# Kernel optimization log

Measured on AMD Instinct MI355X. Metric: run time of the kernel, lower is better.

The kernel has to match this reference:

```python
import jax, jax.numpy as jnp
import numpy as np

N = 100000   # nodes
E = 1600000  # edges (before self-loops)
IN, H, HID, OUT = 128, 4, 32, 16
G, NPG = 100, 1000  # graphs, nodes per graph
NEG_SLOPE = 0.2


def setup_inputs() -> dict:
    key = jax.random.key(0)
    ks = jax.random.split(key, 12)
    x = jax.random.normal(ks[0], (N, IN), dtype=jnp.float32)
    # node type in column 0: first node of each graph is the root (type 0)
    node_type = (jnp.arange(N) % NPG != 0).astype(jnp.float32)
    x = x.at[:, 0].set(node_type)
    edge_index = jax.random.randint(ks[1], (2, E), 0, N, dtype=jnp.int64)
    batch = (jnp.arange(N) // NPG).astype(jnp.int64)
    s = 0.1
    W1 = jax.random.normal(ks[2], (IN, H * HID), dtype=jnp.float32) * s
    att_src1 = jax.random.normal(ks[3], (H, HID), dtype=jnp.float32) * s
    att_dst1 = jax.random.normal(ks[4], (H, HID), dtype=jnp.float32) * s
    bias1 = jnp.zeros((H * HID,), dtype=jnp.float32)
    W2 = jax.random.normal(ks[5], (H * HID, OUT), dtype=jnp.float32) * s
    att_src2 = jax.random.normal(ks[6], (1, OUT), dtype=jnp.float32) * s
    att_dst2 = jax.random.normal(ks[7], (1, OUT), dtype=jnp.float32) * s
    bias2 = jnp.zeros((OUT,), dtype=jnp.float32)
    return {"x": x, "edge_index": edge_index, "batch": batch,
            "W1": W1, "att_src1": att_src1, "att_dst1": att_dst1, "bias1": bias1,
            "W2": W2, "att_src2": att_src2, "att_dst2": att_dst2, "bias2": bias2}


def gat_conv(x, src, dst, W, att_src, att_dst, bias, heads, out_ch, concat):
    n = x.shape[0]
    h = (x @ W).reshape(n, heads, out_ch)           # [N,H,C]
    a_src = jnp.einsum('nhc,hc->nh', h, att_src)    # [N,H]
    a_dst = jnp.einsum('nhc,hc->nh', h, att_dst)
    e = a_src[src] + a_dst[dst]                     # [E',H]
    e = jnp.where(e > 0, e, NEG_SLOPE * e)          # leaky_relu(0.2)
    # segment softmax over incoming edges of each dst node
    m = jax.ops.segment_max(e, dst, num_segments=n)
    e = jnp.exp(e - m[dst])
    denom = jax.ops.segment_sum(e, dst, num_segments=n)
    alpha = e / (denom[dst] + 1e-16)                # [E',H]
    msg = h[src] * alpha[:, :, None]                # [E',H,C]
    out = jax.ops.segment_sum(msg, dst, num_segments=n)  # [N,H,C]
    if concat:
        return out.reshape(n, heads * out_ch) + bias
    return out.mean(axis=1) + bias


def reference(x, edge_index, batch, W1, att_src1, att_dst1, bias1,
              W2, att_src2, att_dst2, bias2):
    # eval mode: feature/attention dropout are identity
    ar = jnp.arange(N, dtype=edge_index.dtype)
    ei = jnp.concatenate([edge_index, jnp.stack([ar, ar])], axis=1)  # add self-loops
    src, dst = ei[0], ei[1]
    h = gat_conv(x, src, dst, W1, att_src1, att_dst1, bias1, H, HID, True)
    h = jax.nn.elu(h)
    out = gat_conv(h, src, dst, W2, att_src2, att_dst2, bias2, 1, OUT, False)
    # first root (node_type==0) per graph
    node_types = x[:, 0]
    cand = jnp.where(node_types == 0, jnp.arange(N), N)
    roots = jax.ops.segment_min(cand, batch, num_segments=G)
    return out[roots]
```

## Files before the change

kernel.cpp:

```cpp
#include <hip/hip_runtime.h>
#include <math.h>

#define NN 100000
#define EE 1600000
#define GG 100
#define DIN 128
#define F1 128
#define FOUT 16

#define C1CAP 16384
#define C0CAP 49152
#define L2CAP 32768
#define DEGCAP 128
#define NT 16

#define O_CNT      0
#define O_FLAG1    (O_CNT + 8)
#define O_FLAG0    (O_FLAG1 + NN)
#define O_ISROOT   (O_FLAG0 + NN)
#define O_FILL     (O_ISROOT + NN)
#define O_ZEND     (O_FILL + C1CAP)
#define O_ROOT     (O_ZEND)
#define O_MAP1     (O_ROOT + GG)
#define O_MAP0     (O_MAP1 + NN)
#define O_LIST1    (O_MAP0 + NN)
#define O_LIST0    (O_LIST1 + C1CAP)
#define O_L2       (O_LIST0 + C0CAP)
#define O_ORDER    (O_L2 + L2CAP*2)
#define O_H1       (O_ORDER + C1CAP*DEGCAP)
#define O_A1S      (O_H1 + C0CAP*F1)
#define O_A1D      (O_A1S + C0CAP*4)
#define O_H2       (O_A1D + C0CAP*4)
#define O_A2S      (O_H2 + C1CAP*FOUT)
#define O_A2D      (O_A2S + C1CAP)
#define O_END      (O_A2D + C1CAP)

__global__ __launch_bounds__(256) void gat_roots(
    const float* __restrict__ x, const int* __restrict__ batch, int* ws) {
  int i = blockIdx.x * blockDim.x + threadIdx.x;
  if (i < NN && x[(size_t)i * DIN] == 0.f)
    atomicMin((unsigned int*)&ws[O_ROOT + batch[i]], (unsigned int)i);
  __threadfence();
  __syncthreads();
  __shared__ int lastFlag;
  if (threadIdx.x == 0)
    lastFlag = (atomicAdd(&ws[O_CNT + 7], 1) == (int)gridDim.x - 1);
  __syncthreads();
  if (!lastFlag) return;
  int g = threadIdx.x;
  if (g >= GG) return;
  unsigned int r = __hip_atomic_load((unsigned int*)&ws[O_ROOT + g],
                                     __ATOMIC_ACQUIRE, __HIP_MEMORY_SCOPE_AGENT);
  if (r >= NN) return;
  ws[O_ISROOT + r] = g + 1;
  ws[O_FLAG1 + r] = 1;
  int idx = atomicAdd(&ws[O_CNT + 0], 1);
  if (idx < C1CAP) {
    ws[O_MAP1 + r] = idx;
    ws[O_LIST1 + idx] = r;
    ws[O_FILL + idx] = 1;
    ws[O_ORDER + idx * DEGCAP] = (int)r;
  }
  int p = atomicAdd(&ws[O_CNT + 3], 1);
  if (p < L2CAP) { ws[O_L2 + 2*p] = (int)r; ws[O_L2 + 2*p + 1] = g; }
  ws[O_FLAG0 + r] = 1;
  int i0 = atomicAdd(&ws[O_CNT + 1], 1);
  if (i0 < C0CAP) { ws[O_MAP0 + r] = i0; ws[O_LIST0 + i0] = (int)r; }
}

#define SB2 1600
__global__ __launch_bounds__(256) void gat_scan2(const int* __restrict__ ei, int* __restrict__ ws) {
  __shared__ int sp[SB2 * 2];
  __shared__ int sc[SB2];
  __shared__ int nP, nC, bP, bC, b0;
  if (threadIdx.x == 0) { nP = 0; nC = 0; }
  __syncthreads();
  const int perBlock = (EE + gridDim.x - 1) / gridDim.x;
  const int beg = blockIdx.x * perBlock;
  const int end = min(beg + perBlock, EE);
  for (int e = beg + threadIdx.x; e < end; e += 256) {
    int d = ei[EE + e];
    int gi = ws[O_ISROOT + d];
    if (gi) {
      int s = ei[e];
      int p = atomicAdd(&nP, 1);
      sp[2*p] = s; sp[2*p + 1] = gi - 1;
      if (atomicCAS(&ws[O_FLAG1 + s], 0, 1) == 0)
        sc[atomicAdd(&nC, 1)] = s;
    }
  }
  __syncthreads();
  if (threadIdx.x == 0) {
    bP = nP ? atomicAdd(&ws[O_CNT + 3], nP) : 0;
    bC = nC ? atomicAdd(&ws[O_CNT + 0], nC) : 0;
    b0 = nC ? atomicAdd(&ws[O_CNT + 1], nC) : 0;
  }
  __syncthreads();
  for (int i = threadIdx.x; i < nP; i += 256) {
    int p = bP + i;
    if (p < L2CAP) { ws[O_L2 + 2*p] = sp[2*i]; ws[O_L2 + 2*p + 1] = sp[2*i + 1]; }
  }
  for (int i = threadIdx.x; i < nC; i += 256) {
    int node = sc[i], idx = bC + i, i0 = b0 + i;
    if (idx < C1CAP) {
      ws[O_MAP1 + node] = idx;
      ws[O_LIST1 + idx] = node;
      ws[O_FILL + idx] = 1;
      ws[O_ORDER + idx * DEGCAP] = node;
    }
    ws[O_FLAG0 + node] = 1;
    if (i0 < C0CAP) { ws[O_MAP0 + node] = i0; ws[O_LIST0 + i0] = node; }
  }
}

__global__ __launch_bounds__(256) void gat_scan1(const int* __restrict__ ei, int* __restrict__ ws) {
  __shared__ int sc[SB2];
  __shared__ int nC, b0;
  if (threadIdx.x == 0) nC = 0;
  __syncthreads();
  const int perBlock = (EE + gridDim.x - 1) / gridDim.x;
  const int beg = blockIdx.x * perBlock;
  const int end = min(beg + perBlock, EE);
  for (int e = beg + threadIdx.x; e < end; e += 256) {
    int d = ei[EE + e];
    if (ws[O_FLAG1 + d]) {
      int s = ei[e];
      int md1 = ws[O_MAP1 + d];
      if ((unsigned)md1 < C1CAP) {
        int pos = atomicAdd(&ws[O_FILL + md1], 1);
        if (pos < DEGCAP) ws[O_ORDER + md1 * DEGCAP + pos] = s;
      }
      if (atomicCAS(&ws[O_FLAG0 + s], 0, 1) == 0)
        sc[atomicAdd(&nC, 1)] = s;
    }
  }
  __syncthreads();
  if (threadIdx.x == 0) b0 = nC ? atomicAdd(&ws[O_CNT + 1], nC) : 0;
  __syncthreads();
  for (int i = threadIdx.x; i < nC; i += 256) {
    int node = sc[i], i0 = b0 + i;
    if (i0 < C0CAP) { ws[O_MAP0 + node] = i0; ws[O_LIST0 + i0] = node; }
  }
}

__global__ __launch_bounds__(256) void gat_h1lin(
    const float* __restrict__ x, const float* __restrict__ W1,
    const float* __restrict__ att_s1, const float* __restrict__ att_d1, int* ws) {
  __shared__ float xs[NT][DIN];
  int t = threadIdx.x, col = t & 127, half = t >> 7;
  int c0 = ws[O_CNT + 1]; if (c0 > C0CAP) c0 = C0CAP;
  float* h1  = (float*)(ws + O_H1);
  float* a1s = (float*)(ws + O_A1S);
  float* a1d = (float*)(ws + O_A1D);
  float as1v = att_s1[col], ad1v = att_d1[col];
  for (int tile = blockIdx.x * NT; tile < c0; tile += gridDim.x * NT) {
    {
      int n = t >> 4, k0 = (t & 15) * 8;
      int ci = tile + n;
      if (ci < c0) {
        int v = ws[O_LIST0 + ci];
        const float4* src = (const float4*)&x[(size_t)v * DIN + k0];
        *(float4*)&xs[n][k0]     = src[0];
        *(float4*)&xs[n][k0 + 4] = src[1];
      }
    }
    __syncthreads();
    float acc[8];
    #pragma unroll
    for (int i = 0; i < 8; ++i) acc[i] = 0.f;
    #pragma unroll 4
    for (int k = 0; k < DIN; k += 4) {
      float w0 = W1[(k + 0) * F1 + col];
      float w1 = W1[(k + 1) * F1 + col];
      float w2 = W1[(k + 2) * F1 + col];
      float w3 = W1[(k + 3) * F1 + col];
      #pragma unroll
      for (int n8 = 0; n8 < 8; ++n8) {
        const float4 xv = *(const float4*)&xs[half * 8 + n8][k];
        acc[n8] = fmaf(xv.x, w0, acc[n8]);
        acc[n8] = fmaf(xv.y, w1, acc[n8]);
        acc[n8] = fmaf(xv.z, w2, acc[n8]);
        acc[n8] = fmaf(xv.w, w3, acc[n8]);
      }
    }
    #pragma unroll
    for (int n8 = 0; n8 < 8; ++n8) {
      int ci = tile + half * 8 + n8;
      bool ok = ci < c0;
      if (ok) h1[(size_t)ci * F1 + col] = acc[n8];
      float cs = acc[n8] * as1v, cd = acc[n8] * ad1v;
      #pragma unroll
      for (int off = 16; off > 0; off >>= 1) {
        cs += __shfl_down(cs, off, 32);
        cd += __shfl_down(cd, off, 32);
      }
      if (ok && (col & 31) == 0) {
        a1s[ci * 4 + (col >> 5)] = cs;
        a1d[ci * 4 + (col >> 5)] = cd;
      }
    }
    __syncthreads();
  }
}

__global__ __launch_bounds__(256) void gat_e1agg(
    const float* __restrict__ b1, const float* __restrict__ W2,
    const float* __restrict__ att_s2, const float* __restrict__ att_d2, int* ws) {
  int c1 = ws[O_CNT + 0]; if (c1 > C1CAP) c1 = C1CAP;
  float* a1s = (float*)(ws + O_A1S);
  float* a1d = (float*)(ws + O_A1D);
  float* h1  = (float*)(ws + O_H1);
  float* h2  = (float*)(ws + O_H2);
  float* a2s = (float*)(ws + O_A2S);
  float* a2d = (float*)(ws + O_A2D);
  __shared__ int   msBuf[DEGCAP];
  __shared__ float wBuf[DEGCAP * 4];
  __shared__ float sacc[2][F1];
  __shared__ float hs[F1];
  __shared__ float s1L[4];
  __shared__ float h2row[FOUT];
  int t = threadIdx.x, col = t & 127, half = t >> 7;
  for (int ci = blockIdx.x; ci < c1; ci += gridDim.x) {
    int cnt = ws[O_FILL + ci]; if (cnt > DEGCAP) cnt = DEGCAP;
    int node = ws[O_LIST1 + ci];
    int md0 = ws[O_MAP0 + node]; if ((unsigned)md0 >= C0CAP) md0 = 0;
    if (t < cnt) {
      int srcn = ws[O_ORDER + ci * DEGCAP + t];
      int ms = ws[O_MAP0 + srcn]; if ((unsigned)ms >= C0CAP) ms = 0;
      msBuf[t] = ms;
      #pragma unroll
      for (int h = 0; h < 4; ++h) {
        float ev = a1s[ms * 4 + h] + a1d[md0 * 4 + h];
        ev = ev > 0.f ? ev : 0.2f * ev;
        wBuf[t * 4 + h] = __expf(ev);
      }
    }
    __syncthreads();
    float acc = 0.f;
    for (int j = half; j < cnt; j += 2)
      acc = fmaf(h1[(size_t)msBuf[j] * F1 + col], wBuf[j * 4 + (col >> 5)], acc);
    sacc[half][col] = acc;
    if (t < 4) { float sh = 0.f; for (int j = 0; j < cnt; ++j) sh += wBuf[j * 4 + t]; s1L[t] = sh; }
    __syncthreads();
    if (half == 0) {
      float hv = (sacc[0][col] + sacc[1][col]) / (s1L[col >> 5] + 1e-16f) + b1[col];
      hs[col] = hv > 0.f ? hv : (__expf(hv) - 1.f);
    }
    __syncthreads();
    {
      int o = t >> 4, r = t & 15;
      float p = 0.f;
      for (int c = r; c < F1; c += 16) p = fmaf(hs[c], W2[c * FOUT + o], p);
      #pragma unroll
      for (int off = 8; off > 0; off >>= 1) p += __shfl_down(p, off, 16);
      if (r == 0) { h2[(size_t)ci * FOUT + o] = p; h2row[o] = p; }
    }
    __syncthreads();
    if (t < 2) {
      const float* av = t ? att_d2 : att_s2;
      float s = 0.f;
      #pragma unroll
      for (int o = 0; o < FOUT; ++o) s += h2row[o] * av[o];
      if (t == 0) a2s[ci] = s; else a2d[ci] = s;
    }
    __syncthreads();
  }
}

__global__ __launch_bounds__(256) void gat_e2out(
    const float* __restrict__ b2, int* ws, float* __restrict__ out) {
  __shared__ float acc2[GG * FOUT];
  __shared__ float sL[GG];
  __shared__ float a2dR[GG];
  __shared__ float wE[2048];
  int t = threadIdx.x;
  float* a2s = (float*)(ws + O_A2S);
  float* a2d = (float*)(ws + O_A2D);
  float* h2  = (float*)(ws + O_H2);
  int l2 = ws[O_CNT + 3]; if (l2 > L2CAP) l2 = L2CAP;
  for (int i = t; i < GG * FOUT; i += 256) acc2[i] = 0.f;
  for (int i = t; i < GG; i += 256) {
    sL[i] = 0.f;
    unsigned int r = (unsigned int)ws[O_ROOT + i];
    int m = (r < NN) ? ws[O_MAP1 + (int)r] : 0;
    if ((unsigned)m >= C1CAP) m = 0;
    a2dR[i] = a2d[m];
  }
  __syncthreads();
  for (int cb = 0; cb < l2; cb += 2048) {
    int cc = min(2048, l2 - cb);
    for (int i = t; i < cc; i += 256) {
      int s = ws[O_L2 + 2*(cb + i)], g = ws[O_L2 + 2*(cb + i) + 1];
      int msi = ws[O_MAP1 + s]; if ((unsigned)msi >= C1CAP) msi = 0;
      float e = a2s[msi] + a2dR[g];
      e = e > 0.f ? e : 0.2f * e;
      float w = __expf(e);
      wE[i] = w;
      atomicAdd(&sL[g], w);
    }
    __syncthreads();
    for (int idx = t; idx < cc * FOUT; idx += 256) {
      int i = idx >> 4, o = idx & 15;
      int s = ws[O_L2 + 2*(cb + i)], g = ws[O_L2 + 2*(cb + i) + 1];
      int msi = ws[O_MAP1 + s]; if ((unsigned)msi >= C1CAP) msi = 0;
      atomicAdd(&acc2[g * FOUT + o], h2[(size_t)msi * FOUT + o] * wE[i]);
    }
    __syncthreads();
  }
  for (int i = t; i < GG * FOUT; i += 256) {
    int g = i >> 4, o = i & 15;
    out[i] = acc2[i] / (sL[g] + 1e-16f) + b2[o];
  }
}

extern "C" void kernel_launch(void* const* d_in, const int* in_sizes, int n_in,
                              void* d_out, int out_size, void* d_ws, size_t ws_size,
                              hipStream_t stream) {
  const float* x    = (const float*)d_in[0];
  const int*   ei   = (const int*)d_in[1];
  const int*   batch= (const int*)d_in[2];
  const float* W1   = (const float*)d_in[3];
  const float* as1  = (const float*)d_in[4];
  const float* ad1  = (const float*)d_in[5];
  const float* b1   = (const float*)d_in[6];
  const float* W2   = (const float*)d_in[7];
  const float* as2  = (const float*)d_in[8];
  const float* ad2  = (const float*)d_in[9];
  const float* b2   = (const float*)d_in[10];
  float* out = (float*)d_out;
  int* ws = (int*)d_ws;

  hipMemsetAsync(ws, 0, (size_t)O_ZEND * 4, stream);
  hipMemsetAsync(ws + O_ROOT, 0xFF, (size_t)GG * 4, stream);
  gat_roots<<<(NN + 255) / 256, 256, 0, stream>>>(x, batch, ws);
  gat_scan2<<<1024, 256, 0, stream>>>(ei, ws);
  gat_scan1<<<1024, 256, 0, stream>>>(ei, ws);
  gat_h1lin<<<C0CAP / NT, 256, 0, stream>>>(x, W1, as1, ad1, ws);
  gat_e1agg<<<2048, 256, 0, stream>>>(b1, W2, as2, ad2, ws);
  gat_e2out<<<1, 256, 0, stream>>>(b2, ws, out);
}
```

Measured before the change: 307.0 us.

## Parallelize final layer-2 root aggregation across many blocks with last-block reduction

The final layer-2 aggregation over root-incident edges moves from a single block to 256 blocks. Each block accumulates into shared memory, then atomically adds its partials to global buffers that are zeroed with the existing memset. A counter picks the last block to finish, and that block normalizes and writes the output. This removes the serial single-block bottleneck, at the cost of global atomics and a threadfence-based completion scheme.

```diff
diff --git a/kernel.cpp b/kernel.cpp
--- a/kernel.cpp
+++ b/kernel.cpp
@@ -19,7 +19,9 @@
 #define O_FLAG0    (O_FLAG1 + NN)
 #define O_ISROOT   (O_FLAG0 + NN)
 #define O_FILL     (O_ISROOT + NN)
-#define O_ZEND     (O_FILL + C1CAP)
+#define O_ACC2     (O_FILL + C1CAP)
+#define O_SL       (O_ACC2 + GG*FOUT)
+#define O_ZEND     (O_SL + GG)
 #define O_ROOT     (O_ZEND)
 #define O_MAP1     (O_ROOT + GG)
 #define O_MAP0     (O_MAP1 + NN)
@@ -267,16 +269,19 @@
   }
 }
 
+#define E2CH 64
 __global__ __launch_bounds__(256) void gat_e2out(
     const float* __restrict__ b2, int* ws, float* __restrict__ out) {
   __shared__ float acc2[GG * FOUT];
   __shared__ float sL[GG];
   __shared__ float a2dR[GG];
-  __shared__ float wE[2048];
+  __shared__ int lastFlag;
   int t = threadIdx.x;
-  float* a2s = (float*)(ws + O_A2S);
-  float* a2d = (float*)(ws + O_A2D);
-  float* h2  = (float*)(ws + O_H2);
+  float* a2s  = (float*)(ws + O_A2S);
+  float* a2d  = (float*)(ws + O_A2D);
+  float* h2   = (float*)(ws + O_H2);
+  float* gacc = (float*)(ws + O_ACC2);
+  float* gsl  = (float*)(ws + O_SL);
   int l2 = ws[O_CNT + 3]; if (l2 > L2CAP) l2 = L2CAP;
   for (int i = t; i < GG * FOUT; i += 256) acc2[i] = 0.f;
   for (int i = t; i < GG; i += 256) {
@@ -287,29 +292,41 @@
     a2dR[i] = a2d[m];
   }
   __syncthreads();
-  for (int cb = 0; cb < l2; cb += 2048) {
-    int cc = min(2048, l2 - cb);
-    for (int i = t; i < cc; i += 256) {
-      int s = ws[O_L2 + 2*(cb + i)], g = ws[O_L2 + 2*(cb + i) + 1];
+  bool touched = false;
+  int pi = t & 63, sub = t >> 6;
+  for (int base = blockIdx.x * E2CH; base < l2; base += gridDim.x * E2CH) {
+    int i = base + pi;
+    if (pi < E2CH && i < l2) {
+      int s = ws[O_L2 + 2*i], g = ws[O_L2 + 2*i + 1];
       int msi = ws[O_MAP1 + s]; if ((unsigned)msi >= C1CAP) msi = 0;
       float e = a2s[msi] + a2dR[g];
       e = e > 0.f ? e : 0.2f * e;
       float w = __expf(e);
-      wE[i] = w;
-      atomicAdd(&sL[g], w);
-    }
-    __syncthreads();
-    for (int idx = t; idx < cc * FOUT; idx += 256) {
-      int i = idx >> 4, o = idx & 15;
-      int s = ws[O_L2 + 2*(cb + i)], g = ws[O_L2 + 2*(cb + i) + 1];
-      int msi = ws[O_MAP1 + s]; if ((unsigned)msi >= C1CAP) msi = 0;
-      atomicAdd(&acc2[g * FOUT + o], h2[(size_t)msi * FOUT + o] * wE[i]);
-    }
-    __syncthreads();
-  }
+      if (sub == 0) atomicAdd(&sL[g], w);
+      #pragma unroll
+      for (int oo = 0; oo < 4; ++oo) {
+        int o = sub * 4 + oo;
+        atomicAdd(&acc2[g * FOUT + o], h2[(size_t)msi * FOUT + o] * w);
+      }
+      touched = true;
+    }
+  }
+  __syncthreads();
+  if (__syncthreads_or(touched)) {
+    for (int i = t; i < GG * FOUT; i += 256) atomicAdd(&gacc[i], acc2[i]);
+    for (int i = t; i < GG; i += 256) atomicAdd(&gsl[i], sL[i]);
+  }
+  __threadfence();
+  __syncthreads();
+  if (t == 0)
+    lastFlag = (atomicAdd(&ws[O_CNT + 6], 1) == (int)gridDim.x - 1);
+  __syncthreads();
+  if (!lastFlag) return;
   for (int i = t; i < GG * FOUT; i += 256) {
     int g = i >> 4, o = i & 15;
-    out[i] = acc2[i] / (sL[g] + 1e-16f) + b2[o];
+    float a = __hip_atomic_load(&gacc[i], __ATOMIC_ACQUIRE, __HIP_MEMORY_SCOPE_AGENT);
+    float sden = __hip_atomic_load(&gsl[g], __ATOMIC_ACQUIRE, __HIP_MEMORY_SCOPE_AGENT);
+    out[i] = a / (sden + 1e-16f) + b2[o];
   }
 }
 
@@ -337,5 +354,5 @@
   gat_scan1<<<1024, 256, 0, stream>>>(ei, ws);
   gat_h1lin<<<C0CAP / NT, 256, 0, stream>>>(x, W1, as1, ad1, ws);
   gat_e1agg<<<2048, 256, 0, stream>>>(b1, W2, as2, ad2, ws);
-  gat_e2out<<<1, 256, 0, stream>>>(b2, ws, out);
-}
+  gat_e2out<<<256, 256, 0, stream>>>(b2, ws, out);
+}
```

Measured after the change: 274.2 us. 10.7% less time.
